# Performance work log

Hardware: AMD Instinct MI355X
Metric: run time of the kernel (lower is better)

The kernel has to match this reference:

```python
import jax, jax.numpy as jnp
import numpy as np

N_NODES = 50000
N_EDGES = 800000
D_IN = 128
D_HID = 128
BN_EPS = 1e-5


def _sage_mean(h, src, dst, w_self, w_neigh, b):
    # DGL SAGEConv('mean'): out = h @ W_self + mean_{neighbors}(h_src) @ W_neigh + bias
    msg = h[src]                                               # [E, D] gather
    ssum = jax.ops.segment_sum(msg, dst, num_segments=N_NODES)  # [N, D]
    deg = jax.ops.segment_sum(jnp.ones((src.shape[0],), h.dtype), dst,
                              num_segments=N_NODES)            # [N]
    mean = ssum / jnp.maximum(deg, 1.0)[:, None]
    return h @ w_self + mean @ w_neigh + b


def _bn_relu(h, gamma, beta):
    # BatchNorm1d with batch statistics (training-mode math), then ReLU.
    m = jnp.mean(h, axis=0)
    v = jnp.mean(jnp.square(h - m), axis=0)  # biased variance, as torch uses for normalization
    hn = (h - m) * jax.lax.rsqrt(v + BN_EPS) * gamma + beta
    return jax.nn.relu(hn)


def setup_inputs() -> dict:
    key = jax.random.key(0)
    ks = jax.random.split(key, 16)
    x = jax.random.normal(ks[0], (N_NODES, D_IN), dtype=jnp.float32)
    src = jax.random.randint(ks[1], (N_EDGES,), 0, N_NODES, dtype=jnp.int32)
    dst = jax.random.randint(ks[2], (N_EDGES,), 0, N_NODES, dtype=jnp.int32)
    s0 = 1.0 / np.sqrt(D_IN)
    s1 = 1.0 / np.sqrt(D_HID)
    inp = {
        'x': x, 'src': src, 'dst': dst,
        'W_self0': jax.random.uniform(ks[3], (D_IN, D_HID), jnp.float32, -s0, s0),
        'W_neigh0': jax.random.uniform(ks[4], (D_IN, D_HID), jnp.float32, -s0, s0),
        'b0': jnp.zeros((D_HID,), jnp.float32),
        'W_self1': jax.random.uniform(ks[5], (D_HID, D_HID), jnp.float32, -s1, s1),
        'W_neigh1': jax.random.uniform(ks[6], (D_HID, D_HID), jnp.float32, -s1, s1),
        'b1': jnp.zeros((D_HID,), jnp.float32),
        'W_self2': jax.random.uniform(ks[7], (D_HID, D_HID), jnp.float32, -s1, s1),
        'W_neigh2': jax.random.uniform(ks[8], (D_HID, D_HID), jnp.float32, -s1, s1),
        'b2': jnp.zeros((D_HID,), jnp.float32),
        'gamma0': jnp.ones((D_HID,), jnp.float32),
        'beta0': jnp.zeros((D_HID,), jnp.float32),
        'gamma1': jnp.ones((D_HID,), jnp.float32),
        'beta1': jnp.zeros((D_HID,), jnp.float32),
    }
    return inp


def reference(x, src, dst,
              W_self0, W_neigh0, b0,
              W_self1, W_neigh1, b1,
              W_self2, W_neigh2, b2,
              gamma0, beta0, gamma1, beta1):
    h = _sage_mean(x, src, dst, W_self0, W_neigh0, b0)
    h = _bn_relu(h, gamma0, beta0)  # dropout is identity in eval mode
    h = _sage_mean(h, src, dst, W_self1, W_neigh1, b1)
    h = _bn_relu(h, gamma1, beta1)
    h = _sage_mean(h, src, dst, W_self2, W_neigh2, b2)
    return h
```

## Files before the change

kernel.cpp:

```cpp
#include <hip/hip_runtime.h>

#define N_NODES 50000
#define N_EDGES 800000
#define D 128
#define BN_EPS 1e-5f

#define NBUCK 391
#define BSHIFT 7
#define S1_BLOCKS 256
#define EPB 3125
#define CVT_BLOCKS 6250
#define PACK_BLOCKS 384
#define NREP 16
#define NSLICE 8
#define SSHIFT 13
#define BN_BLOCKS 512

typedef __attribute__((ext_vector_type(8))) short bf16x8;
typedef __attribute__((ext_vector_type(4))) float f32x4;

__device__ inline unsigned short f2bf(float f) {
    unsigned int u = __float_as_uint(f);
    u = (u + 0x7FFF + ((u >> 16) & 1)) >> 16;
    return (unsigned short)u;
}

__device__ inline float bf2f(unsigned short b) {
    return __uint_as_float(((unsigned)b) << 16);
}

__device__ __forceinline__ void acc_plain(float* a, uint4 v) {
    unsigned w[4] = {v.x, v.y, v.z, v.w};
#pragma unroll
    for (int p = 0; p < 4; p++) {
        a[2 * p]     += __uint_as_float(w[p] << 16);
        a[2 * p + 1] += __uint_as_float(w[p] & 0xffff0000u);
    }
}


__global__ void fused_prep(const float* __restrict__ x, unsigned short* __restrict__ x16,
                           const int* __restrict__ dst, int* __restrict__ hist,
                           const float* __restrict__ Ws0, const float* __restrict__ Wn0,
                           const float* __restrict__ Ws1, const float* __restrict__ Wn1,
                           const float* __restrict__ Ws2, const float* __restrict__ Wn2,
                           unsigned short* __restrict__ Wf, float* __restrict__ statsg) {
    __shared__ int lh[NBUCK];
    const int bid = blockIdx.x, t = threadIdx.x;

    if (bid < CVT_BLOCKS) {
        int idx = bid * 256 + t;
        float4 v = ((const float4*)x)[idx];
        ushort4 o;
        o.x = f2bf(v.x); o.y = f2bf(v.y); o.z = f2bf(v.z); o.w = f2bf(v.w);
        ((ushort4*)x16)[idx] = o;
    } else if (bid < CVT_BLOCKS + S1_BLOCKS) {
        int blk = bid - CVT_BLOCKS;
        for (int i = t; i < NBUCK; i += 256) lh[i] = 0;
        __syncthreads();
        int e0 = blk * EPB;
        for (int i = 0; i < 13; i++) {
            int k = t + i * 256;
            if (k < EPB) atomicAdd(&lh[dst[e0 + k] >> BSHIFT], 1);
        }
        __syncthreads();
        for (int i = t; i < NBUCK; i += 256) hist[blk * NBUCK + i] = lh[i];
    } else {
        if (bid == CVT_BLOCKS + S1_BLOCKS) {
            for (int i = t; i < 2 * NREP * 256; i += 256) statsg[i] = 0.f;
        }
        int idx = (bid - (CVT_BLOCKS + S1_BLOCKS)) * 256 + t;
        if (idx < 3 * 32768) {
            int layer = idx >> 15;
            int rem = idx & 32767;
            int kt = rem >> 12;
            int nt = (rem >> 9) & 7;
            int lane = (rem >> 3) & 63;
            int j = rem & 7;
            int k = kt * 32 + (lane >> 4) * 8 + j;
            int n = nt * 16 + (lane & 15);
            const float* Wsrc;
            if (layer == 0) Wsrc = (k < 128) ? Ws0 : Wn0;
            else if (layer == 1) Wsrc = (k < 128) ? Ws1 : Wn1;
            else Wsrc = (k < 128) ? Ws2 : Wn2;
            Wf[idx] = f2bf(Wsrc[(k & 127) * D + n]);
        }
    }
}


__global__ void s2a(int* __restrict__ hist, int* __restrict__ bucketTotal) {
    __shared__ int s[S1_BLOCKS];
    int b = blockIdx.x, t = threadIdx.x;
    int v = hist[t * NBUCK + b];
    s[t] = v;
    __syncthreads();
    for (int off = 1; off < S1_BLOCKS; off <<= 1) {
        int x = (t >= off) ? s[t - off] : 0;
        __syncthreads();
        s[t] += x;
        __syncthreads();
    }
    hist[t * NBUCK + b] = s[t] - v;
    if (t == S1_BLOCKS - 1) bucketTotal[b] = s[t];
}


__global__ void s3_scatter(const int* __restrict__ src, const int* __restrict__ dst,
                           const int* __restrict__ hist, const int* __restrict__ bucketTotal,
                           int* __restrict__ bucketStart, unsigned int* __restrict__ rec) {
    __shared__ int sc[512];
    __shared__ int base[NBUCK];
    int blk = blockIdx.x, t = threadIdx.x;
    int i1 = t + 256;
    int v0 = (t < NBUCK) ? bucketTotal[t] : 0;
    int v1 = (i1 < NBUCK) ? bucketTotal[i1] : 0;
    sc[t] = v0; sc[i1] = v1;
    __syncthreads();
    for (int off = 1; off < 512; off <<= 1) {
        int x0 = (t >= off) ? sc[t - off] : 0;
        int x1 = (i1 >= off) ? sc[i1 - off] : 0;
        __syncthreads();
        sc[t] += x0; sc[i1] += x1;
        __syncthreads();
    }
    if (t < NBUCK)  base[t]  = (sc[t] - v0)  + hist[blk * NBUCK + t];
    if (i1 < NBUCK) base[i1] = (sc[i1] - v1) + hist[blk * NBUCK + i1];
    if (blk == 0) {
        if (t < NBUCK)  bucketStart[t]  = sc[t] - v0;
        if (i1 < NBUCK) bucketStart[i1] = sc[i1] - v1;
        if (t == 0) bucketStart[NBUCK] = N_EDGES;
    }
    __syncthreads();
    int e0 = blk * EPB;
    for (int i = 0; i < 13; i++) {
        int k = t + i * 256;
        if (k < EPB) {
            int e = e0 + k;
            int d = dst[e];
            int p = atomicAdd(&base[d >> BSHIFT], 1);
            rec[p] = ((unsigned)(d & 127) << 16) | (unsigned)src[e];
        }
    }
}


__global__ void s4_build(const unsigned int* __restrict__ rec, const int* __restrict__ bucketStart,
                         unsigned short* __restrict__ csr, int* __restrict__ degi,
                         int* __restrict__ offsets, float* __restrict__ inv_deg) {
    __shared__ int cnt[128 * NSLICE];
    __shared__ int exc[128 * NSLICE];
    __shared__ int lcur[128 * NSLICE];
    __shared__ int ls[256];
    int b = blockIdx.x, t = threadIdx.x;
    int start = bucketStart[b], end = bucketStart[b + 1];

    for (int i = t; i < 128 * NSLICE; i += 256) cnt[i] = 0;
    __syncthreads();
    for (int e = start + t; e < end; e += 256) {
        unsigned r = rec[e];
        int key = ((r >> 16) << 3) | ((r & 0xFFFFu) >> SSHIFT);
        atomicAdd(&cnt[key], 1);
    }
    __syncthreads();

    int c0 = cnt[4 * t], c1 = cnt[4 * t + 1], c2 = cnt[4 * t + 2], c3 = cnt[4 * t + 3];
    int sum4 = c0 + c1 + c2 + c3;
    ls[t] = sum4;
    __syncthreads();
    for (int off = 1; off < 256; off <<= 1) {
        int x = (t >= off) ? ls[t - off] : 0;
        __syncthreads();
        ls[t] += x;
        __syncthreads();
    }
    int base = ls[t] - sum4;
    exc[4 * t]     = base;
    exc[4 * t + 1] = base + c0;
    exc[4 * t + 2] = base + c0 + c1;
    exc[4 * t + 3] = base + c0 + c1 + c2;
    lcur[4 * t]     = start + base;
    lcur[4 * t + 1] = start + base + c0;
    lcur[4 * t + 2] = start + base + c0 + c1;
    lcur[4 * t + 3] = start + base + c0 + c1 + c2;
    __syncthreads();

    if (t < 128) {
        int node = (b << BSHIFT) + t;
        int e0 = exc[8 * t];
        int e1 = (t == 127) ? (end - start) : exc[8 * t + 8];
        int v = e1 - e0;
        if (node < N_NODES) {
            degi[node] = v;
            offsets[node] = start + e0;
            inv_deg[node] = 1.0f / (float)max(v, 1);
        }
    }
    __syncthreads();
    for (int e = start + t; e < end; e += 256) {
        unsigned r = rec[e];
        int key = ((r >> 16) << 3) | ((r & 0xFFFFu) >> SSHIFT);
        int p = atomicAdd(&lcur[key], 1);
        csr[p] = (unsigned short)(r & 0xFFFFu);
    }
}


__global__ void bn_relu_apply(unsigned short* __restrict__ h,
                              const float* __restrict__ stats,
                              const float* __restrict__ gamma, const float* __restrict__ beta) {
    __shared__ float sc[128], sh[128];
    int t = threadIdx.x;
    if (t < 128) {
        const float invN = 1.0f / (float)N_NODES;
        float s = 0.f, q = 0.f;
#pragma unroll
        for (int r = 0; r < NREP; r++) {
            s += stats[r * 256 + t];
            q += stats[r * 256 + 128 + t];
        }
        float m = s * invN;
        float var = q * invN - m * m;
        float scv = rsqrtf(var + BN_EPS) * gamma[t];
        sc[t] = scv;
        sh[t] = beta[t] - m * scv;
    }
    __syncthreads();
    const int total = N_NODES * D / 8;
    for (int idx = blockIdx.x * 256 + t; idx < total; idx += BN_BLOCKS * 256) {
        uint4 v = ((const uint4*)h)[idx];
        int col0 = (idx & 15) * 8;
        unsigned w[4] = {v.x, v.y, v.z, v.w};
        unsigned ow[4];
#pragma unroll
        for (int p = 0; p < 4; p++) {
            float lo = __uint_as_float(w[p] << 16);
            float hi = __uint_as_float(w[p] & 0xffff0000u);
            float rlo = fmaxf(lo * sc[col0 + 2 * p]     + sh[col0 + 2 * p],     0.f);
            float rhi = fmaxf(hi * sc[col0 + 2 * p + 1] + sh[col0 + 2 * p + 1], 0.f);
            ow[p] = ((unsigned)f2bf(rhi) << 16) | f2bf(rlo);
        }
        uint4 o;
        o.x = ow[0]; o.y = ow[1]; o.z = ow[2]; o.w = ow[3];
        ((uint4*)h)[idx] = o;
    }
}


#define GATHER(k) (*(const uint4*)(h16 + (size_t)csr[beg + (k)] * D + c * 8))

__global__ void aggregate16(const unsigned short* __restrict__ h16,
                            const unsigned short* __restrict__ csr, const int* __restrict__ offsets,
                            const int* __restrict__ degi, const float* __restrict__ inv_deg,
                            unsigned short* __restrict__ mean16) {
    int t = threadIdx.x;
    int node = blockIdx.x * 16 + (t >> 4);
    if (node >= N_NODES) return;
    int c = t & 15;
    int beg = offsets[node], n = degi[node];
    float a[8];
#pragma unroll
    for (int j = 0; j < 8; j++) a[j] = 0.f;

    int i = 0;
    if (n >= 4) {
        uint4 v0 = GATHER(0), v1 = GATHER(1), v2 = GATHER(2), v3 = GATHER(3);
        for (i = 4; i + 3 < n; i += 4) {
            uint4 w0 = GATHER(i), w1 = GATHER(i + 1), w2 = GATHER(i + 2), w3 = GATHER(i + 3);
            acc_plain(a, v0); acc_plain(a, v1); acc_plain(a, v2); acc_plain(a, v3);
            v0 = w0; v1 = w1; v2 = w2; v3 = w3;
        }
        acc_plain(a, v0); acc_plain(a, v1); acc_plain(a, v2); acc_plain(a, v3);
    }
    for (; i < n; i++) { uint4 v = GATHER(i); acc_plain(a, v); }

    float w = inv_deg[node];
    uint4 o;
    o.x = ((unsigned)f2bf(a[1] * w) << 16) | f2bf(a[0] * w);
    o.y = ((unsigned)f2bf(a[3] * w) << 16) | f2bf(a[2] * w);
    o.z = ((unsigned)f2bf(a[5] * w) << 16) | f2bf(a[4] * w);
    o.w = ((unsigned)f2bf(a[7] * w) << 16) | f2bf(a[6] * w);
    *(uint4*)(mean16 + (size_t)node * D + c * 8) = o;
}


__global__ __launch_bounds__(256, 4) void sage_gemm(
    const unsigned short* __restrict__ h16, const unsigned short* __restrict__ mean16,
    const unsigned short* __restrict__ Wf, const float* __restrict__ bias,
    unsigned short* __restrict__ out16, float* __restrict__ outf,
    float* __restrict__ statsOut) {
    __shared__ unsigned short sWf[16384];
    __shared__ float sstat[256];
    const int t = threadIdx.x;
    const int lane = t & 63;
    const int m = lane & 15;
    const int quad = lane >> 4;
    const int wrow0 = blockIdx.x * 64 + (t >> 6) * 16;

    int arow = wrow0 + m;
    if (arow >= N_NODES) arow = N_NODES - 1;

    bf16x8 afr[8];
#pragma unroll
    for (int kt = 0; kt < 4; kt++)
        afr[kt] = *(const bf16x8*)(h16 + (size_t)arow * D + kt * 32 + quad * 8);
#pragma unroll
    for (int kt = 0; kt < 4; kt++)
        afr[4 + kt] = *(const bf16x8*)(mean16 + (size_t)arow * D + kt * 32 + quad * 8);

    const uint4* W4 = (const uint4*)Wf;
    uint4* S4 = (uint4*)sWf;
#pragma unroll
    for (int i = 0; i < 8; i++) S4[i * 256 + t] = W4[i * 256 + t];
    if (statsOut) sstat[t] = 0.f;
    __syncthreads();

    f32x4 acc[8];
#pragma unroll
    for (int i = 0; i < 8; i++) acc[i] = (f32x4)(0.f);

#pragma unroll
    for (int kt = 0; kt < 4; kt++) {
#pragma unroll
        for (int nt = 0; nt < 8; nt++) {
            bf16x8 bf = *(const bf16x8*)(sWf + ((kt * 8 + nt) * 64 + lane) * 8);
            acc[nt] = __builtin_amdgcn_mfma_f32_16x16x32_bf16(afr[kt], bf, acc[nt], 0, 0, 0);
        }
    }

    __syncthreads();
#pragma unroll
    for (int i = 0; i < 8; i++) S4[i * 256 + t] = W4[2048 + i * 256 + t];
    __syncthreads();

#pragma unroll
    for (int kt = 4; kt < 8; kt++) {
#pragma unroll
        for (int nt = 0; nt < 8; nt++) {
            bf16x8 bf = *(const bf16x8*)(sWf + (((kt - 4) * 8 + nt) * 64 + lane) * 8);
            acc[nt] = __builtin_amdgcn_mfma_f32_16x16x32_bf16(afr[kt], bf, acc[nt], 0, 0, 0);
        }
    }

    const bool do16 = (out16 != nullptr);
#pragma unroll
    for (int nt = 0; nt < 8; nt++) {
        int cidx = nt * 16 + m;
        float bv = bias[cidx];
        float s = 0.f, q = 0.f;
#pragma unroll
        for (int reg = 0; reg < 4; reg++) {
            int r = wrow0 + quad * 4 + reg;
            float v = acc[nt][reg] + bv;
            if (r < N_NODES) {
                if (do16) out16[(size_t)r * D + cidx] = f2bf(v);
                else      outf[(size_t)r * D + cidx] = v;
                s += v; q += v * v;
            }
        }
        if (statsOut) {
            s += __shfl_xor(s, 16); s += __shfl_xor(s, 32);
            q += __shfl_xor(q, 16); q += __shfl_xor(q, 32);
            if (quad == 0) {
                atomicAdd(&sstat[cidx], s);
                atomicAdd(&sstat[128 + cidx], q);
            }
        }
    }
    if (statsOut) {
        __syncthreads();
        atomicAdd(&statsOut[(blockIdx.x & (NREP - 1)) * 256 + t], sstat[t]);
    }
}


extern "C" void kernel_launch(void* const* d_in, const int* in_sizes, int n_in,
                              void* d_out, int out_size, void* d_ws, size_t ws_size,
                              hipStream_t stream) {
    const float* x   = (const float*)d_in[0];
    const int* src   = (const int*)d_in[1];
    const int* dst   = (const int*)d_in[2];
    const float* Ws0 = (const float*)d_in[3];
    const float* Wn0 = (const float*)d_in[4];
    const float* b0  = (const float*)d_in[5];
    const float* Ws1 = (const float*)d_in[6];
    const float* Wn1 = (const float*)d_in[7];
    const float* b1  = (const float*)d_in[8];
    const float* Ws2 = (const float*)d_in[9];
    const float* Wn2 = (const float*)d_in[10];
    const float* b2  = (const float*)d_in[11];
    const float* g0  = (const float*)d_in[12];
    const float* be0 = (const float*)d_in[13];
    const float* g1  = (const float*)d_in[14];
    const float* be1 = (const float*)d_in[15];

    char* base = (char*)d_ws;
    size_t NND = (size_t)N_NODES * D;
    unsigned short* X16    = (unsigned short*)base;
    unsigned short* H16    = (unsigned short*)(base + NND * 2);
    unsigned short* mean16 = (unsigned short*)(base + 2 * NND * 2);
    char* p = base + 6 * NND;
    unsigned short* Wf = (unsigned short*)p;  p += 3 * 32768 * 2;
    int* hist          = (int*)p;             p += (size_t)S1_BLOCKS * NBUCK * 4;
    int* bucketTotal   = (int*)p;             p += 1568;
    int* bucketStart   = (int*)p;             p += 1600;
    unsigned int* rec  = (unsigned int*)p;    p += (size_t)N_EDGES * 4;
    unsigned short* csr = (unsigned short*)p; p += (size_t)N_EDGES * 2;
    int* degi    = (int*)p;                   p += N_NODES * 4;
    int* offsets = (int*)p;                   p += N_NODES * 4;
    float* inv_deg = (float*)p;               p += N_NODES * 4;
    float* stats   = (float*)p;               p += 2 * NREP * 256 * 4;
    float* stats0 = stats, *stats1 = stats + NREP * 256;

    fused_prep<<<CVT_BLOCKS + S1_BLOCKS + PACK_BLOCKS, 256, 0, stream>>>(
        x, X16, dst, hist, Ws0, Wn0, Ws1, Wn1, Ws2, Wn2, Wf, stats);
    s2a<<<NBUCK, 256, 0, stream>>>(hist, bucketTotal);
    s3_scatter<<<S1_BLOCKS, 256, 0, stream>>>(src, dst, hist, bucketTotal, bucketStart, rec);
    s4_build<<<NBUCK, 256, 0, stream>>>(rec, bucketStart, csr, degi, offsets, inv_deg);

    const int AGG_B = (N_NODES + 15) / 16;
    const int GEMM_B = (N_NODES + 63) / 64;

    aggregate16<<<AGG_B, 256, 0, stream>>>(X16, csr, offsets, degi, inv_deg, mean16);
    sage_gemm<<<GEMM_B, 256, 0, stream>>>(X16, mean16, Wf, b0, H16, nullptr, stats0);

    bn_relu_apply<<<BN_BLOCKS, 256, 0, stream>>>(H16, stats0, g0, be0);
    aggregate16<<<AGG_B, 256, 0, stream>>>(H16, csr, offsets, degi, inv_deg, mean16);
    sage_gemm<<<GEMM_B, 256, 0, stream>>>(H16, mean16, Wf + 32768, b1, X16, nullptr, stats1);

    bn_relu_apply<<<BN_BLOCKS, 256, 0, stream>>>(X16, stats1, g1, be1);
    aggregate16<<<AGG_B, 256, 0, stream>>>(X16, csr, offsets, degi, inv_deg, mean16);
    sage_gemm<<<GEMM_B, 256, 0, stream>>>(X16, mean16, Wf + 65536, b2, nullptr,
                                          (float*)d_out, nullptr);
}
```

Measured before the change: 279.6 us.

## Process aggregation nodes in degree-sorted order and use packed float2 accumulation

A new single-block kernel counting-sorts nodes by in-degree, highest first, into a permutation. The aggregation kernel then walks nodes in that order, so the four nodes sharing a wavefront have similar neighbour counts and lanes diverge less. The accumulator becomes float2 vectors so the compiler can emit packed adds. The cost is an extra serial launch, an extra indirection per thread, and output rows written in scattered order.

Result: slower. 312.9 us (+11.9%).

```diff
diff --git a/kernel.cpp b/kernel.cpp
--- a/kernel.cpp
+++ b/kernel.cpp
@@ -18,6 +18,7 @@
 
 typedef __attribute__((ext_vector_type(8))) short bf16x8;
 typedef __attribute__((ext_vector_type(4))) float f32x4;
+typedef __attribute__((ext_vector_type(2))) float f32x2;
 
 __device__ inline unsigned short f2bf(float f) {
     unsigned int u = __float_as_uint(f);
@@ -29,12 +30,14 @@
     return __uint_as_float(((unsigned)b) << 16);
 }
 
-__device__ __forceinline__ void acc_plain(float* a, uint4 v) {
+__device__ __forceinline__ void acc_plain(f32x2* a, uint4 v) {
     unsigned w[4] = {v.x, v.y, v.z, v.w};
 #pragma unroll
     for (int p = 0; p < 4; p++) {
-        a[2 * p]     += __uint_as_float(w[p] << 16);
-        a[2 * p + 1] += __uint_as_float(w[p] & 0xffff0000u);
+        f32x2 f;
+        f.x = __uint_as_float(w[p] << 16);
+        f.y = __uint_as_float(w[p] & 0xffff0000u);
+        a[p] += f;
     }
 }
 
@@ -206,6 +209,32 @@
 }
 
 
+__global__ void degsort(const int* __restrict__ degi, int* __restrict__ perm) {
+    __shared__ int h[256];
+    __shared__ int cur[256];
+    int t = threadIdx.x;
+    if (t < 256) h[t] = 0;
+    __syncthreads();
+    for (int i = t; i < N_NODES; i += 1024)
+        atomicAdd(&h[255 - min(degi[i], 255)], 1);
+    __syncthreads();
+    int v = (t < 256) ? h[t] : 0;
+    for (int off = 1; off < 256; off <<= 1) {
+        int x = 0;
+        if (t < 256 && t >= off) x = h[t - off];
+        __syncthreads();
+        if (t < 256) h[t] += x;
+        __syncthreads();
+    }
+    if (t < 256) cur[t] = h[t] - v;
+    __syncthreads();
+    for (int i = t; i < N_NODES; i += 1024) {
+        int b = 255 - min(degi[i], 255);
+        perm[atomicAdd(&cur[b], 1)] = i;
+    }
+}
+
+
 __global__ void bn_relu_apply(unsigned short* __restrict__ h,
                               const float* __restrict__ stats,
                               const float* __restrict__ gamma, const float* __restrict__ beta) {
@@ -247,20 +276,21 @@
 }
 
 
-#define GATHER(k) (*(const uint4*)(h16 + (size_t)csr[beg + (k)] * D + c * 8))
+#define GATHER(k) (*(const uint4*)(hb + ((size_t)csr[beg + (k)] << 7)))
 
 __global__ void aggregate16(const unsigned short* __restrict__ h16,
                             const unsigned short* __restrict__ csr, const int* __restrict__ offsets,
                             const int* __restrict__ degi, const float* __restrict__ inv_deg,
+                            const int* __restrict__ perm,
                             unsigned short* __restrict__ mean16) {
     int t = threadIdx.x;
-    int node = blockIdx.x * 16 + (t >> 4);
-    if (node >= N_NODES) return;
+    int node = perm[blockIdx.x * 16 + (t >> 4)];
     int c = t & 15;
+    const unsigned short* hb = h16 + c * 8;
     int beg = offsets[node], n = degi[node];
-    float a[8];
-#pragma unroll
-    for (int j = 0; j < 8; j++) a[j] = 0.f;
+    f32x2 a[4];
+#pragma unroll
+    for (int j = 0; j < 4; j++) a[j] = (f32x2)(0.f);
 
     int i = 0;
     if (n >= 4) {
@@ -276,10 +306,10 @@
 
     float w = inv_deg[node];
     uint4 o;
-    o.x = ((unsigned)f2bf(a[1] * w) << 16) | f2bf(a[0] * w);
-    o.y = ((unsigned)f2bf(a[3] * w) << 16) | f2bf(a[2] * w);
-    o.z = ((unsigned)f2bf(a[5] * w) << 16) | f2bf(a[4] * w);
-    o.w = ((unsigned)f2bf(a[7] * w) << 16) | f2bf(a[6] * w);
+    o.x = ((unsigned)f2bf(a[0].y * w) << 16) | f2bf(a[0].x * w);
+    o.y = ((unsigned)f2bf(a[1].y * w) << 16) | f2bf(a[1].x * w);
+    o.z = ((unsigned)f2bf(a[2].y * w) << 16) | f2bf(a[2].x * w);
+    o.w = ((unsigned)f2bf(a[3].y * w) << 16) | f2bf(a[3].x * w);
     *(uint4*)(mean16 + (size_t)node * D + c * 8) = o;
 }
 
@@ -409,6 +439,7 @@
     int* degi    = (int*)p;                   p += N_NODES * 4;
     int* offsets = (int*)p;                   p += N_NODES * 4;
     float* inv_deg = (float*)p;               p += N_NODES * 4;
+    int* perm    = (int*)p;                   p += N_NODES * 4;
     float* stats   = (float*)p;               p += 2 * NREP * 256 * 4;
     float* stats0 = stats, *stats1 = stats + NREP * 256;
 
@@ -417,19 +448,20 @@
     s2a<<<NBUCK, 256, 0, stream>>>(hist, bucketTotal);
     s3_scatter<<<S1_BLOCKS, 256, 0, stream>>>(src, dst, hist, bucketTotal, bucketStart, rec);
     s4_build<<<NBUCK, 256, 0, stream>>>(rec, bucketStart, csr, degi, offsets, inv_deg);
+    degsort<<<1, 1024, 0, stream>>>(degi, perm);
 
     const int AGG_B = (N_NODES + 15) / 16;
     const int GEMM_B = (N_NODES + 63) / 64;
 
-    aggregate16<<<AGG_B, 256, 0, stream>>>(X16, csr, offsets, degi, inv_deg, mean16);
+    aggregate16<<<AGG_B, 256, 0, stream>>>(X16, csr, offsets, degi, inv_deg, perm, mean16);
     sage_gemm<<<GEMM_B, 256, 0, stream>>>(X16, mean16, Wf, b0, H16, nullptr, stats0);
 
     bn_relu_apply<<<BN_BLOCKS, 256, 0, stream>>>(H16, stats0, g0, be0);
-    aggregate16<<<AGG_B, 256, 0, stream>>>(H16, csr, offsets, degi, inv_deg, mean16);
+    aggregate16<<<AGG_B, 256, 0, stream>>>(H16, csr, offsets, degi, inv_deg, perm, mean16);
     sage_gemm<<<GEMM_B, 256, 0, stream>>>(H16, mean16, Wf + 32768, b1, X16, nullptr, stats1);
 
     bn_relu_apply<<<BN_BLOCKS, 256, 0, stream>>>(X16, stats1, g1, be1);
-    aggregate16<<<AGG_B, 256, 0, stream>>>(X16, csr, offsets, degi, inv_deg, mean16);
+    aggregate16<<<AGG_B, 256, 0, stream>>>(X16, csr, offsets, degi, inv_deg, perm, mean16);
     sage_gemm<<<GEMM_B, 256, 0, stream>>>(X16, mean16, Wf + 65536, b2, nullptr,
                                           (float*)d_out, nullptr);
 }
```

## Split each node's neighbor gather across four edge groups per wavefront

Applied to the files above, without the earlier changes.

The mean-aggregation kernel now gives each node a full 64-lane wavefront instead of 16 lanes. Four groups of 16 lanes each take every fourth neighbor and keep three loads in flight, and the partial sums are combined with cross-lane shuffles before one group writes the result. Accumulators become float2 vectors so the compiler can use packed adds. This raises memory-level parallelism for the latency-bound gathers at average degree 16, at the cost of more blocks, lanes idling on low-degree nodes, and shuffle overhead.

New measurement: 294.8 us. +5.4%, slower.

```diff
diff --git a/kernel.cpp b/kernel.cpp
--- a/kernel.cpp
+++ b/kernel.cpp
@@ -18,6 +18,7 @@
 
 typedef __attribute__((ext_vector_type(8))) short bf16x8;
 typedef __attribute__((ext_vector_type(4))) float f32x4;
+typedef __attribute__((ext_vector_type(2))) float f32x2;
 
 __device__ inline unsigned short f2bf(float f) {
     unsigned int u = __float_as_uint(f);
@@ -29,12 +30,14 @@
     return __uint_as_float(((unsigned)b) << 16);
 }
 
-__device__ __forceinline__ void acc_plain(float* a, uint4 v) {
+__device__ __forceinline__ void acc_plain(f32x2* a, uint4 v) {
     unsigned w[4] = {v.x, v.y, v.z, v.w};
 #pragma unroll
     for (int p = 0; p < 4; p++) {
-        a[2 * p]     += __uint_as_float(w[p] << 16);
-        a[2 * p + 1] += __uint_as_float(w[p] & 0xffff0000u);
+        f32x2 f;
+        f.x = __uint_as_float(w[p] << 16);
+        f.y = __uint_as_float(w[p] & 0xffff0000u);
+        a[p] += f;
     }
 }
 
@@ -247,40 +250,56 @@
 }
 
 
-#define GATHER(k) (*(const uint4*)(h16 + (size_t)csr[beg + (k)] * D + c * 8))
+#define GATHER(k) (*(const uint4*)(hb + ((size_t)csr[beg + (k)] << 7)))
 
 __global__ void aggregate16(const unsigned short* __restrict__ h16,
                             const unsigned short* __restrict__ csr, const int* __restrict__ offsets,
                             const int* __restrict__ degi, const float* __restrict__ inv_deg,
                             unsigned short* __restrict__ mean16) {
     int t = threadIdx.x;
-    int node = blockIdx.x * 16 + (t >> 4);
-    if (node >= N_NODES) return;
-    int c = t & 15;
+    int node = blockIdx.x * 4 + (t >> 6);
+    int lane = t & 63;
+    int grp = lane >> 4;
+    int c = lane & 15;
+    const unsigned short* hb = h16 + c * 8;
     int beg = offsets[node], n = degi[node];
-    float a[8];
-#pragma unroll
-    for (int j = 0; j < 8; j++) a[j] = 0.f;
-
-    int i = 0;
-    if (n >= 4) {
-        uint4 v0 = GATHER(0), v1 = GATHER(1), v2 = GATHER(2), v3 = GATHER(3);
-        for (i = 4; i + 3 < n; i += 4) {
-            uint4 w0 = GATHER(i), w1 = GATHER(i + 1), w2 = GATHER(i + 2), w3 = GATHER(i + 3);
-            acc_plain(a, v0); acc_plain(a, v1); acc_plain(a, v2); acc_plain(a, v3);
-            v0 = w0; v1 = w1; v2 = w2; v3 = w3;
-        }
-        acc_plain(a, v0); acc_plain(a, v1); acc_plain(a, v2); acc_plain(a, v3);
-    }
-    for (; i < n; i++) { uint4 v = GATHER(i); acc_plain(a, v); }
-
-    float w = inv_deg[node];
-    uint4 o;
-    o.x = ((unsigned)f2bf(a[1] * w) << 16) | f2bf(a[0] * w);
-    o.y = ((unsigned)f2bf(a[3] * w) << 16) | f2bf(a[2] * w);
-    o.z = ((unsigned)f2bf(a[5] * w) << 16) | f2bf(a[4] * w);
-    o.w = ((unsigned)f2bf(a[7] * w) << 16) | f2bf(a[6] * w);
-    *(uint4*)(mean16 + (size_t)node * D + c * 8) = o;
+    f32x2 a[4];
+#pragma unroll
+    for (int j = 0; j < 4; j++) a[j] = (f32x2)(0.f);
+
+    int rem = n - grp;
+    if (rem > 0) {
+        uint4 v0, v1, v2;
+        v0 = GATHER(grp);
+        if (rem > 4) v1 = GATHER(grp + 4);
+        if (rem > 8) v2 = GATHER(grp + 8);
+        for (int k = grp + 12; k < n; k += 4) {
+            uint4 w = GATHER(k);
+            acc_plain(a, v0);
+            v0 = v1; v1 = v2; v2 = w;
+        }
+        acc_plain(a, v0);
+        if (rem > 4) acc_plain(a, v1);
+        if (rem > 8) acc_plain(a, v2);
+    }
+
+#pragma unroll
+    for (int j = 0; j < 4; j++) {
+        a[j].x += __shfl_xor(a[j].x, 16);
+        a[j].y += __shfl_xor(a[j].y, 16);
+        a[j].x += __shfl_xor(a[j].x, 32);
+        a[j].y += __shfl_xor(a[j].y, 32);
+    }
+
+    if (grp == 0) {
+        float w = inv_deg[node];
+        uint4 o;
+        o.x = ((unsigned)f2bf(a[0].y * w) << 16) | f2bf(a[0].x * w);
+        o.y = ((unsigned)f2bf(a[1].y * w) << 16) | f2bf(a[1].x * w);
+        o.z = ((unsigned)f2bf(a[2].y * w) << 16) | f2bf(a[2].x * w);
+        o.w = ((unsigned)f2bf(a[3].y * w) << 16) | f2bf(a[3].x * w);
+        *(uint4*)(mean16 + (size_t)node * D + c * 8) = o;
+    }
 }
 
 
@@ -418,7 +437,7 @@
     s3_scatter<<<S1_BLOCKS, 256, 0, stream>>>(src, dst, hist, bucketTotal, bucketStart, rec);
     s4_build<<<NBUCK, 256, 0, stream>>>(rec, bucketStart, csr, degi, offsets, inv_deg);
 
-    const int AGG_B = (N_NODES + 15) / 16;
+    const int AGG_B = N_NODES / 4;
     const int GEMM_B = (N_NODES + 63) / 64;
 
     aggregate16<<<AGG_B, 256, 0, stream>>>(X16, csr, offsets, degi, inv_deg, mean16);
```
